# Performance work log

Measured on AMD Instinct MI355X. Metric: run time of the kernel, lower is better.

Reference implementation:

```python
import jax, jax.numpy as jnp
import numpy as np

B, N, T, D = 8, 64, 50, 4      # batch, atoms, timesteps, features per node
K, H = 2, 64                   # edge types, hidden (msg_hid = msg_out = n_hid)
START = 1                      # skip_first_edge_type=True
E = N * (N - 1)


def setup_inputs() -> dict:
    key = jax.random.key(0)
    ks = jax.random.split(key, 10)
    # fully-connected relation graph: all ordered pairs i != j
    recv_idx, send_idx = np.where(~np.eye(N, dtype=bool))
    eye = np.eye(N, dtype=np.float32)
    rel_rec = jnp.asarray(eye[recv_idx])    # [E, N] one-hot receivers
    rel_send = jnp.asarray(eye[send_idx])   # [E, N] one-hot senders
    s = 0.1
    return {
        "inputs": jax.random.normal(ks[0], (B, N, T, D), jnp.float32),
        "rel_type": jax.random.uniform(ks[1], (B, 1, E, K), jnp.float32),
        "rel_rec": rel_rec,
        "rel_send": rel_send,
        "fc1_w": jax.random.normal(ks[2], (K, H, 2 * D), jnp.float32) * s,
        "fc1_b": jnp.zeros((K, H), jnp.float32),
        "fc2_w": jax.random.normal(ks[3], (K, H, H), jnp.float32) * s,
        "fc2_b": jnp.zeros((K, H), jnp.float32),
        "out1_w": jax.random.normal(ks[4], (H, D + H), jnp.float32) * s,
        "out1_b": jnp.zeros((H,), jnp.float32),
        "out2_w": jax.random.normal(ks[5], (H, H), jnp.float32) * s,
        "out2_b": jnp.zeros((H,), jnp.float32),
        "out3_w": jax.random.normal(ks[6], (D, H), jnp.float32) * s,
        "out3_b": jnp.zeros((D,), jnp.float32),
        "pred_steps": 1,
    }


def reference(inputs, rel_type, rel_rec, rel_send,
              fc1_w, fc1_b, fc2_w, fc2_b,
              out1_w, out1_b, out2_w, out2_b, out3_w, out3_b,
              pred_steps):
    assert pred_steps == 1
    x_in = jnp.swapaxes(inputs, 1, 2)  # [B, T, N, D]
    t = x_in.shape[1]
    # rel_type [B,1,E,K] -> expand over time
    rt = jnp.broadcast_to(rel_type, (rel_type.shape[0], t) + rel_type.shape[2:])

    # node2edge: gather receivers/senders via one-hot matmuls
    recv = jnp.einsum('en,btnd->bted', rel_rec, x_in)
    send = jnp.einsum('en,btnd->bted', rel_send, x_in)
    pre_msg = jnp.concatenate([recv, send], axis=-1)  # [B,T,E,2D]

    # per-edge-type MLP, masked by inferred edge prob, accumulated
    all_msgs = jnp.zeros(pre_msg.shape[:3] + (H,), pre_msg.dtype)
    for i in range(START, K):
        h = jax.nn.relu(jnp.einsum('bted,hd->bteh', pre_msg, fc1_w[i]) + fc1_b[i])
        m = jax.nn.relu(jnp.einsum('bteh,oh->bteo', h, fc2_w[i]) + fc2_b[i])
        all_msgs = all_msgs + m * rt[..., i:i + 1]

    # edge2node: scatter-accumulate to receivers via one-hot transpose matmul
    agg = jnp.einsum('en,bteh->btnh', rel_rec, all_msgs)  # [B,T,N,H]

    aug = jnp.concatenate([x_in, agg], axis=-1)           # [B,T,N,D+H]
    h = jax.nn.relu(jnp.einsum('btni,oi->btno', aug, out1_w) + out1_b)
    h = jax.nn.relu(jnp.einsum('btni,oi->btno', h, out2_w) + out2_b)
    delta = jnp.einsum('btni,oi->btno', h, out3_w) + out3_b
    x_tp1 = x_in + delta                                  # predict_delta=True

    pred_all = x_tp1[:, :t - 1]                           # [B,T-1,N,D]
    return jnp.swapaxes(pred_all, 1, 2)                   # [B,N,T-1,D]
```

## Files before the change

kernel.cpp:

```cpp
#include <hip/hip_runtime.h>


#define NB 8
#define NN 64
#define NT 50
#define NTO 49
#define ND 4
#define NH 64
#define NE 4032

typedef _Float16 f16x8 __attribute__((ext_vector_type(8)));
typedef float f32x4 __attribute__((ext_vector_type(4)));

union Frag { unsigned u[4]; f16x8 f; };

__device__ __forceinline__ unsigned pk16(float lo, float hi) {
  return __builtin_bit_cast(unsigned, __builtin_amdgcn_cvt_pkrtz(lo, hi));
}

#define MFMA16(A, B, C) __builtin_amdgcn_mfma_f32_16x16x32_f16((A), (B), (C), 0, 0, 0)

__global__ __launch_bounds__(256) void nri_fused_kernel(
    const float* __restrict__ inputs,
    const float* __restrict__ rel_type,
    const float* __restrict__ fc1_w,
    const float* __restrict__ fc1_b,
    const float* __restrict__ fc2_w,
    const float* __restrict__ fc2_b,
    const float* __restrict__ out1_w,
    const float* __restrict__ out1_b,
    const float* __restrict__ out2_w,
    const float* __restrict__ out2_b,
    const float* __restrict__ out3_w,
    const float* __restrict__ out3_b,
    float* __restrict__ out)
{
  __shared__ float  Vl[NN * 68];
  __shared__ float  Pl[16 * 68];
  __shared__ float  Rl[16 * NN];
  __shared__ float4 Xl[16];
  __shared__ float  AggL[16 * 68];
  __shared__ float  H1L[16 * 68];
  __shared__ float  H2L[16 * 68];

  const int bid    = blockIdx.x;
  const int tile   = bid & 3;
  const int t      = (bid >> 2) % NTO;
  const int b      = bid / (4 * NTO);
  const int n_base = tile * 16;
  const int tid  = threadIdx.x;
  const int lane = tid & 63;
  const int w    = tid >> 6;
  const int q    = lane >> 4;
  const int r    = lane & 15;

  {
    const int k = lane;
    const float4 w1r = *(const float4*)(fc1_w + 512 + k * 8);
    const float4 w1s = *(const float4*)(fc1_w + 516 + k * 8);
    const float  b1k = fc1_b[64 + k];
    for (int i = w; i < NN; i += 4) {
      const float4 x = *(const float4*)(inputs + ((b * NN + i) * NT + t) * ND);
      Vl[i * 68 + k] = w1s.x * x.x + w1s.y * x.y + w1s.z * x.z + w1s.w * x.w;
    }
    for (int i = w; i < 16; i += 4) {
      const float4 x = *(const float4*)(inputs + ((b * NN + n_base + i) * NT + t) * ND);
      Pl[i * 68 + k] = b1k + w1r.x * x.x + w1r.y * x.y + w1r.z * x.z + w1r.w * x.w;
    }
  }
  for (int idx = tid; idx < 16 * NN; idx += 256) {
    const int i = idx >> 6, s = idx & 63;
    const int n = n_base + i;
    Rl[idx] = (s == n) ? 0.f
                       : rel_type[(b * NE + n * 63 + (s < n ? s : s - 1)) * 2 + 1];
  }
  if (tid < 16)
    Xl[tid] = *(const float4*)(inputs + ((b * NN + n_base + tid) * NT + t) * ND);

  Frag bfr[4][2];
  float b2l[4];
#pragma unroll
  for (int nt = 0; nt < 4; ++nt) {
    const int o = nt * 16 + r;
    b2l[nt] = fc2_b[64 + o];
#pragma unroll
    for (int ks = 0; ks < 2; ++ks) {
      const float* p = fc2_w + 4096 + o * 64 + ks * 32 + q * 8;
      const float4 c0 = *(const float4*)p;
      const float4 c1 = *(const float4*)(p + 4);
      bfr[nt][ks].u[0] = pk16(c0.x, c0.y);
      bfr[nt][ks].u[1] = pk16(c0.z, c0.w);
      bfr[nt][ks].u[2] = pk16(c1.x, c1.y);
      bfr[nt][ks].u[3] = pk16(c1.z, c1.w);
    }
  }
  __syncthreads();

#pragma unroll 1
  for (int np = 0; np < 4; ++np) {
    const int ni = w * 4 + np;
    float pn[16];
    *(float4*)(pn + 0)  = *(const float4*)(Pl + ni * 68 + q * 8);
    *(float4*)(pn + 4)  = *(const float4*)(Pl + ni * 68 + q * 8 + 4);
    *(float4*)(pn + 8)  = *(const float4*)(Pl + ni * 68 + 32 + q * 8);
    *(float4*)(pn + 12) = *(const float4*)(Pl + ni * 68 + 36 + q * 8);

    float ag0 = 0.f, ag1 = 0.f, ag2 = 0.f, ag3 = 0.f;
#pragma unroll
    for (int st = 0; st < 4; ++st) {
      const int s = st * 16 + r;
      float vv[16];
      *(float4*)(vv + 0)  = *(const float4*)(Vl + s * 68 + q * 8);
      *(float4*)(vv + 4)  = *(const float4*)(Vl + s * 68 + q * 8 + 4);
      *(float4*)(vv + 8)  = *(const float4*)(Vl + s * 68 + 32 + q * 8);
      *(float4*)(vv + 12) = *(const float4*)(Vl + s * 68 + 36 + q * 8);
      float h[16];
#pragma unroll
      for (int j = 0; j < 16; ++j) h[j] = fmaxf(pn[j] + vv[j], 0.f);
      Frag a0, a1;
      a0.u[0] = pk16(h[0],  h[1]);  a0.u[1] = pk16(h[2],  h[3]);
      a0.u[2] = pk16(h[4],  h[5]);  a0.u[3] = pk16(h[6],  h[7]);
      a1.u[0] = pk16(h[8],  h[9]);  a1.u[1] = pk16(h[10], h[11]);
      a1.u[2] = pk16(h[12], h[13]); a1.u[3] = pk16(h[14], h[15]);

      f32x4 d0 = {b2l[0], b2l[0], b2l[0], b2l[0]};
      f32x4 d1 = {b2l[1], b2l[1], b2l[1], b2l[1]};
      f32x4 d2 = {b2l[2], b2l[2], b2l[2], b2l[2]};
      f32x4 d3 = {b2l[3], b2l[3], b2l[3], b2l[3]};
      d0 = MFMA16(a0.f, bfr[0][0].f, d0); d0 = MFMA16(a1.f, bfr[0][1].f, d0);
      d1 = MFMA16(a0.f, bfr[1][0].f, d1); d1 = MFMA16(a1.f, bfr[1][1].f, d1);
      d2 = MFMA16(a0.f, bfr[2][0].f, d2); d2 = MFMA16(a1.f, bfr[2][1].f, d2);
      d3 = MFMA16(a0.f, bfr[3][0].f, d3); d3 = MFMA16(a1.f, bfr[3][1].f, d3);

      const float4 rt4 = *(const float4*)(Rl + ni * NN + st * 16 + q * 4);
      const float rte[4] = {rt4.x, rt4.y, rt4.z, rt4.w};
#pragma unroll
      for (int e = 0; e < 4; ++e) {
        ag0 = fmaf(rte[e], fmaxf(d0[e], 0.f), ag0);
        ag1 = fmaf(rte[e], fmaxf(d1[e], 0.f), ag1);
        ag2 = fmaf(rte[e], fmaxf(d2[e], 0.f), ag2);
        ag3 = fmaf(rte[e], fmaxf(d3[e], 0.f), ag3);
      }
    }
    ag0 += __shfl_xor(ag0, 16); ag0 += __shfl_xor(ag0, 32);
    ag1 += __shfl_xor(ag1, 16); ag1 += __shfl_xor(ag1, 32);
    ag2 += __shfl_xor(ag2, 16); ag2 += __shfl_xor(ag2, 32);
    ag3 += __shfl_xor(ag3, 16); ag3 += __shfl_xor(ag3, 32);
    const float val = (q == 0) ? ag0 : (q == 1) ? ag1 : (q == 2) ? ag2 : ag3;
    AggL[ni * 68 + lane] = val;
  }

  const int o = w * 16 + r;
  Frag B1[2], B2[2];
#pragma unroll
  for (int ks = 0; ks < 2; ++ks) {
    const float* p1 = out1_w + o * 68 + 4 + ks * 32 + q * 8;
    const float4 c0 = *(const float4*)p1;
    const float4 c1 = *(const float4*)(p1 + 4);
    B1[ks].u[0] = pk16(c0.x, c0.y); B1[ks].u[1] = pk16(c0.z, c0.w);
    B1[ks].u[2] = pk16(c1.x, c1.y); B1[ks].u[3] = pk16(c1.z, c1.w);
    const float* p2 = out2_w + o * 64 + ks * 32 + q * 8;
    const float4 e0 = *(const float4*)p2;
    const float4 e1 = *(const float4*)(p2 + 4);
    B2[ks].u[0] = pk16(e0.x, e0.y); B2[ks].u[1] = pk16(e0.z, e0.w);
    B2[ks].u[2] = pk16(e1.x, e1.y); B2[ks].u[3] = pk16(e1.z, e1.w);
  }
  const float4 w1x = *(const float4*)(out1_w + o * 68);
  const float b1o = out1_b[o];
  const float b2o = out2_b[o];
  __syncthreads();

  {
    Frag A[2];
#pragma unroll
    for (int ks = 0; ks < 2; ++ks) {
      const float4 g0 = *(const float4*)(AggL + r * 68 + ks * 32 + q * 8);
      const float4 g1 = *(const float4*)(AggL + r * 68 + ks * 32 + q * 8 + 4);
      A[ks].u[0] = pk16(g0.x, g0.y); A[ks].u[1] = pk16(g0.z, g0.w);
      A[ks].u[2] = pk16(g1.x, g1.y); A[ks].u[3] = pk16(g1.z, g1.w);
    }
    f32x4 d = {b1o, b1o, b1o, b1o};
    d = MFMA16(A[0].f, B1[0].f, d);
    d = MFMA16(A[1].f, B1[1].f, d);
#pragma unroll
    for (int reg = 0; reg < 4; ++reg) {
      const int n = q * 4 + reg;
      const float4 x = Xl[n];
      const float hv = d[reg] + x.x * w1x.x + x.y * w1x.y + x.z * w1x.z + x.w * w1x.w;
      H1L[n * 68 + o] = fmaxf(hv, 0.f);
    }
  }
  __syncthreads();

  {
    Frag A[2];
#pragma unroll
    for (int ks = 0; ks < 2; ++ks) {
      const float4 g0 = *(const float4*)(H1L + r * 68 + ks * 32 + q * 8);
      const float4 g1 = *(const float4*)(H1L + r * 68 + ks * 32 + q * 8 + 4);
      A[ks].u[0] = pk16(g0.x, g0.y); A[ks].u[1] = pk16(g0.z, g0.w);
      A[ks].u[2] = pk16(g1.x, g1.y); A[ks].u[3] = pk16(g1.z, g1.w);
    }
    f32x4 d = {b2o, b2o, b2o, b2o};
    d = MFMA16(A[0].f, B2[0].f, d);
    d = MFMA16(A[1].f, B2[1].f, d);
#pragma unroll
    for (int reg = 0; reg < 4; ++reg) {
      const int n = q * 4 + reg;
      H2L[n * 68 + o] = fmaxf(d[reg], 0.f);
    }
  }
  __syncthreads();

  if (w == 0) {
    Frag B3[2];
#pragma unroll
    for (int ks = 0; ks < 2; ++ks) {
      const float* p3 = out3_w + (r & 3) * 64 + ks * 32 + q * 8;
      float4 c0 = *(const float4*)p3;
      float4 c1 = *(const float4*)(p3 + 4);
      if (r >= 4) { c0 = make_float4(0, 0, 0, 0); c1 = make_float4(0, 0, 0, 0); }
      B3[ks].u[0] = pk16(c0.x, c0.y); B3[ks].u[1] = pk16(c0.z, c0.w);
      B3[ks].u[2] = pk16(c1.x, c1.y); B3[ks].u[3] = pk16(c1.z, c1.w);
    }
    Frag A[2];
#pragma unroll
    for (int ks = 0; ks < 2; ++ks) {
      const float4 g0 = *(const float4*)(H2L + r * 68 + ks * 32 + q * 8);
      const float4 g1 = *(const float4*)(H2L + r * 68 + ks * 32 + q * 8 + 4);
      A[ks].u[0] = pk16(g0.x, g0.y); A[ks].u[1] = pk16(g0.z, g0.w);
      A[ks].u[2] = pk16(g1.x, g1.y); A[ks].u[3] = pk16(g1.z, g1.w);
    }
    const float b3o = (r < 4) ? out3_b[r] : 0.f;
    f32x4 d = {b3o, b3o, b3o, b3o};
    d = MFMA16(A[0].f, B3[0].f, d);
    d = MFMA16(A[1].f, B3[1].f, d);
    if (r < 4) {
      const float* xf = (const float*)Xl;
#pragma unroll
      for (int reg = 0; reg < 4; ++reg) {
        const int n = q * 4 + reg;
        out[((b * NN + n_base + n) * NTO + t) * ND + r] = xf[n * 4 + r] + d[reg];
      }
    }
  }
}

extern "C" void kernel_launch(void* const* d_in, const int* in_sizes, int n_in,
                              void* d_out, int out_size, void* d_ws, size_t ws_size,
                              hipStream_t stream) {
  const float* inputs   = (const float*)d_in[0];
  const float* rel_type = (const float*)d_in[1];
  const float* fc1_w  = (const float*)d_in[4];
  const float* fc1_b  = (const float*)d_in[5];
  const float* fc2_w  = (const float*)d_in[6];
  const float* fc2_b  = (const float*)d_in[7];
  const float* out1_w = (const float*)d_in[8];
  const float* out1_b = (const float*)d_in[9];
  const float* out2_w = (const float*)d_in[10];
  const float* out2_b = (const float*)d_in[11];
  const float* out3_w = (const float*)d_in[12];
  const float* out3_b = (const float*)d_in[13];
  float* out = (float*)d_out;

  nri_fused_kernel<<<NB * NTO * 4, 256, 0, stream>>>(
      inputs, rel_type, fc1_w, fc1_b, fc2_w, fc2_b,
      out1_w, out1_b, out2_w, out2_b, out3_w, out3_b, out);
}
```

Measured before the change: 129.6 us.

## Split node tiles to 4 receivers per block and compute edge hidden in packed fp16

Each block now handles 4 receiver nodes instead of 16, so the grid is four times larger and each wave processes a single receiver with no inner node loop. The first-layer edge activations (sender and receiver projections) are stored in shared memory as fp16 and combined with packed half add and max, which removes the per-element float-to-half conversions. The cost is that every block recomputes the full 64-node sender projection and reloads the weights, four times as often as before. The output MLP now runs 16-row MFMAs with only 4 valid rows, and the fp16 sums add a little rounding error.

```diff
diff --git a/kernel.cpp b/kernel.cpp
--- a/kernel.cpp
+++ b/kernel.cpp
@@ -6,13 +6,13 @@
 #define NT 50
 #define NTO 49
 #define ND 4
-#define NH 64
 #define NE 4032
 
 typedef _Float16 f16x8 __attribute__((ext_vector_type(8)));
+typedef _Float16 f16x2 __attribute__((ext_vector_type(2)));
 typedef float f32x4 __attribute__((ext_vector_type(4)));
 
-union Frag { unsigned u[4]; f16x8 f; };
+union Frag8 { unsigned u[4]; f16x8 f; f16x2 h[4]; };
 
 __device__ __forceinline__ unsigned pk16(float lo, float hi) {
   return __builtin_bit_cast(unsigned, __builtin_amdgcn_cvt_pkrtz(lo, hi));
@@ -35,19 +35,19 @@
     const float* __restrict__ out3_b,
     float* __restrict__ out)
 {
-  __shared__ float  Vl[NN * 68];
-  __shared__ float  Pl[16 * 68];
-  __shared__ float  Rl[16 * NN];
-  __shared__ float4 Xl[16];
-  __shared__ float  AggL[16 * 68];
-  __shared__ float  H1L[16 * 68];
-  __shared__ float  H2L[16 * 68];
+  __shared__ _Float16 Vh[NN * 72];
+  __shared__ _Float16 Ph[4 * 72];
+  __shared__ float    Rl[4 * NN];
+  __shared__ float4   Xl[4];
+  __shared__ float    AggL[16 * 68];
+  __shared__ float    H1L[16 * 68];
+  __shared__ float    H2L[16 * 68];
 
   const int bid    = blockIdx.x;
-  const int tile   = bid & 3;
-  const int t      = (bid >> 2) % NTO;
-  const int b      = bid / (4 * NTO);
-  const int n_base = tile * 16;
+  const int tilei  = bid & 15;
+  const int t      = (bid >> 4) % NTO;
+  const int b      = bid / (16 * NTO);
+  const int n_base = tilei * 4;
   const int tid  = threadIdx.x;
   const int lane = tid & 63;
   const int w    = tid >> 6;
@@ -59,25 +59,27 @@
     const float4 w1r = *(const float4*)(fc1_w + 512 + k * 8);
     const float4 w1s = *(const float4*)(fc1_w + 516 + k * 8);
     const float  b1k = fc1_b[64 + k];
-    for (int i = w; i < NN; i += 4) {
+#pragma unroll 4
+    for (int i = w * 16; i < w * 16 + 16; ++i) {
       const float4 x = *(const float4*)(inputs + ((b * NN + i) * NT + t) * ND);
-      Vl[i * 68 + k] = w1s.x * x.x + w1s.y * x.y + w1s.z * x.z + w1s.w * x.w;
-    }
-    for (int i = w; i < 16; i += 4) {
-      const float4 x = *(const float4*)(inputs + ((b * NN + n_base + i) * NT + t) * ND);
-      Pl[i * 68 + k] = b1k + w1r.x * x.x + w1r.y * x.y + w1r.z * x.z + w1r.w * x.w;
-    }
-  }
-  for (int idx = tid; idx < 16 * NN; idx += 256) {
-    const int i = idx >> 6, s = idx & 63;
+      Vh[i * 72 + k] = (_Float16)(w1s.x*x.x + w1s.y*x.y + w1s.z*x.z + w1s.w*x.w);
+    }
+    {
+      const int n = n_base + w;
+      const float4 x = *(const float4*)(inputs + ((b * NN + n) * NT + t) * ND);
+      Ph[w * 72 + k] = (_Float16)(b1k + w1r.x*x.x + w1r.y*x.y + w1r.z*x.z + w1r.w*x.w);
+    }
+  }
+  {
+    const int i = w, s = lane;
     const int n = n_base + i;
-    Rl[idx] = (s == n) ? 0.f
-                       : rel_type[(b * NE + n * 63 + (s < n ? s : s - 1)) * 2 + 1];
-  }
-  if (tid < 16)
+    Rl[i * NN + s] = (s == n) ? 0.f
+                   : rel_type[(b * NE + n * 63 + (s < n ? s : s - 1)) * 2 + 1];
+  }
+  if (tid < 4)
     Xl[tid] = *(const float4*)(inputs + ((b * NN + n_base + tid) * NT + t) * ND);
 
-  Frag bfr[4][2];
+  Frag8 bfr[4][2];
   float b2l[4];
 #pragma unroll
   for (int nt = 0; nt < 4; ++nt) {
@@ -96,62 +98,57 @@
   }
   __syncthreads();
 
-#pragma unroll 1
-  for (int np = 0; np < 4; ++np) {
-    const int ni = w * 4 + np;
-    float pn[16];
-    *(float4*)(pn + 0)  = *(const float4*)(Pl + ni * 68 + q * 8);
-    *(float4*)(pn + 4)  = *(const float4*)(Pl + ni * 68 + q * 8 + 4);
-    *(float4*)(pn + 8)  = *(const float4*)(Pl + ni * 68 + 32 + q * 8);
-    *(float4*)(pn + 12) = *(const float4*)(Pl + ni * 68 + 36 + q * 8);
-
-    float ag0 = 0.f, ag1 = 0.f, ag2 = 0.f, ag3 = 0.f;
-#pragma unroll
-    for (int st = 0; st < 4; ++st) {
-      const int s = st * 16 + r;
-      float vv[16];
-      *(float4*)(vv + 0)  = *(const float4*)(Vl + s * 68 + q * 8);
-      *(float4*)(vv + 4)  = *(const float4*)(Vl + s * 68 + q * 8 + 4);
-      *(float4*)(vv + 8)  = *(const float4*)(Vl + s * 68 + 32 + q * 8);
-      *(float4*)(vv + 12) = *(const float4*)(Vl + s * 68 + 36 + q * 8);
-      float h[16];
-#pragma unroll
-      for (int j = 0; j < 16; ++j) h[j] = fmaxf(pn[j] + vv[j], 0.f);
-      Frag a0, a1;
-      a0.u[0] = pk16(h[0],  h[1]);  a0.u[1] = pk16(h[2],  h[3]);
-      a0.u[2] = pk16(h[4],  h[5]);  a0.u[3] = pk16(h[6],  h[7]);
-      a1.u[0] = pk16(h[8],  h[9]);  a1.u[1] = pk16(h[10], h[11]);
-      a1.u[2] = pk16(h[12], h[13]); a1.u[3] = pk16(h[14], h[15]);
-
-      f32x4 d0 = {b2l[0], b2l[0], b2l[0], b2l[0]};
-      f32x4 d1 = {b2l[1], b2l[1], b2l[1], b2l[1]};
-      f32x4 d2 = {b2l[2], b2l[2], b2l[2], b2l[2]};
-      f32x4 d3 = {b2l[3], b2l[3], b2l[3], b2l[3]};
-      d0 = MFMA16(a0.f, bfr[0][0].f, d0); d0 = MFMA16(a1.f, bfr[0][1].f, d0);
-      d1 = MFMA16(a0.f, bfr[1][0].f, d1); d1 = MFMA16(a1.f, bfr[1][1].f, d1);
-      d2 = MFMA16(a0.f, bfr[2][0].f, d2); d2 = MFMA16(a1.f, bfr[2][1].f, d2);
-      d3 = MFMA16(a0.f, bfr[3][0].f, d3); d3 = MFMA16(a1.f, bfr[3][1].f, d3);
-
-      const float4 rt4 = *(const float4*)(Rl + ni * NN + st * 16 + q * 4);
-      const float rte[4] = {rt4.x, rt4.y, rt4.z, rt4.w};
-#pragma unroll
-      for (int e = 0; e < 4; ++e) {
-        ag0 = fmaf(rte[e], fmaxf(d0[e], 0.f), ag0);
-        ag1 = fmaf(rte[e], fmaxf(d1[e], 0.f), ag1);
-        ag2 = fmaf(rte[e], fmaxf(d2[e], 0.f), ag2);
-        ag3 = fmaf(rte[e], fmaxf(d3[e], 0.f), ag3);
-      }
-    }
-    ag0 += __shfl_xor(ag0, 16); ag0 += __shfl_xor(ag0, 32);
-    ag1 += __shfl_xor(ag1, 16); ag1 += __shfl_xor(ag1, 32);
-    ag2 += __shfl_xor(ag2, 16); ag2 += __shfl_xor(ag2, 32);
-    ag3 += __shfl_xor(ag3, 16); ag3 += __shfl_xor(ag3, 32);
-    const float val = (q == 0) ? ag0 : (q == 1) ? ag1 : (q == 2) ? ag2 : ag3;
-    AggL[ni * 68 + lane] = val;
-  }
+  const int ni = w;
+  Frag8 pa0, pa1;
+  {
+    const _Float16* pp = Ph + ni * 72 + q * 8;
+    pa0.f = *(const f16x8*)pp;
+    pa1.f = *(const f16x8*)(pp + 32);
+  }
+
+  float ag0 = 0.f, ag1 = 0.f, ag2 = 0.f, ag3 = 0.f;
+#pragma unroll
+  for (int st = 0; st < 4; ++st) {
+    const int s = st * 16 + r;
+    const _Float16* vp = Vh + s * 72 + q * 8;
+    Frag8 va0, va1, a0, a1;
+    va0.f = *(const f16x8*)vp;
+    va1.f = *(const f16x8*)(vp + 32);
+    const f16x2 z = {(_Float16)0.f, (_Float16)0.f};
+#pragma unroll
+    for (int j = 0; j < 4; ++j) {
+      a0.h[j] = __builtin_elementwise_max((f16x2)(pa0.h[j] + va0.h[j]), z);
+      a1.h[j] = __builtin_elementwise_max((f16x2)(pa1.h[j] + va1.h[j]), z);
+    }
+
+    f32x4 d0 = {b2l[0], b2l[0], b2l[0], b2l[0]};
+    f32x4 d1 = {b2l[1], b2l[1], b2l[1], b2l[1]};
+    f32x4 d2 = {b2l[2], b2l[2], b2l[2], b2l[2]};
+    f32x4 d3 = {b2l[3], b2l[3], b2l[3], b2l[3]};
+    d0 = MFMA16(a0.f, bfr[0][0].f, d0); d0 = MFMA16(a1.f, bfr[0][1].f, d0);
+    d1 = MFMA16(a0.f, bfr[1][0].f, d1); d1 = MFMA16(a1.f, bfr[1][1].f, d1);
+    d2 = MFMA16(a0.f, bfr[2][0].f, d2); d2 = MFMA16(a1.f, bfr[2][1].f, d2);
+    d3 = MFMA16(a0.f, bfr[3][0].f, d3); d3 = MFMA16(a1.f, bfr[3][1].f, d3);
+
+    const float4 rt4 = *(const float4*)(Rl + ni * NN + st * 16 + q * 4);
+    const float rte[4] = {rt4.x, rt4.y, rt4.z, rt4.w};
+#pragma unroll
+    for (int e = 0; e < 4; ++e) {
+      ag0 = fmaf(rte[e], fmaxf(d0[e], 0.f), ag0);
+      ag1 = fmaf(rte[e], fmaxf(d1[e], 0.f), ag1);
+      ag2 = fmaf(rte[e], fmaxf(d2[e], 0.f), ag2);
+      ag3 = fmaf(rte[e], fmaxf(d3[e], 0.f), ag3);
+    }
+  }
+  ag0 += __shfl_xor(ag0, 16); ag0 += __shfl_xor(ag0, 32);
+  ag1 += __shfl_xor(ag1, 16); ag1 += __shfl_xor(ag1, 32);
+  ag2 += __shfl_xor(ag2, 16); ag2 += __shfl_xor(ag2, 32);
+  ag3 += __shfl_xor(ag3, 16); ag3 += __shfl_xor(ag3, 32);
+  const float aval = (q == 0) ? ag0 : (q == 1) ? ag1 : (q == 2) ? ag2 : ag3;
+  AggL[ni * 68 + lane] = aval;
 
   const int o = w * 16 + r;
-  Frag B1[2], B2[2];
+  Frag8 B1[2], B2[2];
 #pragma unroll
   for (int ks = 0; ks < 2; ++ks) {
     const float* p1 = out1_w + o * 68 + 4 + ks * 32 + q * 8;
@@ -171,76 +168,81 @@
   __syncthreads();
 
   {
-    Frag A[2];
-#pragma unroll
-    for (int ks = 0; ks < 2; ++ks) {
-      const float4 g0 = *(const float4*)(AggL + r * 68 + ks * 32 + q * 8);
-      const float4 g1 = *(const float4*)(AggL + r * 68 + ks * 32 + q * 8 + 4);
-      A[ks].u[0] = pk16(g0.x, g0.y); A[ks].u[1] = pk16(g0.z, g0.w);
-      A[ks].u[2] = pk16(g1.x, g1.y); A[ks].u[3] = pk16(g1.z, g1.w);
-    }
+    Frag8 A0, A1;
+    const float* gp = AggL + r * 68 + q * 8;
+    const float4 g0 = *(const float4*)gp;
+    const float4 g1 = *(const float4*)(gp + 4);
+    const float4 g2 = *(const float4*)(gp + 32);
+    const float4 g3 = *(const float4*)(gp + 36);
+    A0.u[0] = pk16(g0.x, g0.y); A0.u[1] = pk16(g0.z, g0.w);
+    A0.u[2] = pk16(g1.x, g1.y); A0.u[3] = pk16(g1.z, g1.w);
+    A1.u[0] = pk16(g2.x, g2.y); A1.u[1] = pk16(g2.z, g2.w);
+    A1.u[2] = pk16(g3.x, g3.y); A1.u[3] = pk16(g3.z, g3.w);
     f32x4 d = {b1o, b1o, b1o, b1o};
-    d = MFMA16(A[0].f, B1[0].f, d);
-    d = MFMA16(A[1].f, B1[1].f, d);
-#pragma unroll
-    for (int reg = 0; reg < 4; ++reg) {
-      const int n = q * 4 + reg;
-      const float4 x = Xl[n];
-      const float hv = d[reg] + x.x * w1x.x + x.y * w1x.y + x.z * w1x.z + x.w * w1x.w;
-      H1L[n * 68 + o] = fmaxf(hv, 0.f);
-    }
-  }
-  __syncthreads();
-
-  {
-    Frag A[2];
-#pragma unroll
-    for (int ks = 0; ks < 2; ++ks) {
-      const float4 g0 = *(const float4*)(H1L + r * 68 + ks * 32 + q * 8);
-      const float4 g1 = *(const float4*)(H1L + r * 68 + ks * 32 + q * 8 + 4);
-      A[ks].u[0] = pk16(g0.x, g0.y); A[ks].u[1] = pk16(g0.z, g0.w);
-      A[ks].u[2] = pk16(g1.x, g1.y); A[ks].u[3] = pk16(g1.z, g1.w);
-    }
+    d = MFMA16(A0.f, B1[0].f, d);
+    d = MFMA16(A1.f, B1[1].f, d);
+    if (q == 0) {
+#pragma unroll
+      for (int reg = 0; reg < 4; ++reg) {
+        const float4 x = Xl[reg];
+        const float hv = d[reg] + x.x*w1x.x + x.y*w1x.y + x.z*w1x.z + x.w*w1x.w;
+        H1L[reg * 68 + o] = fmaxf(hv, 0.f);
+      }
+    }
+  }
+  __syncthreads();
+
+  {
+    Frag8 A0, A1;
+    const float* gp = H1L + r * 68 + q * 8;
+    const float4 g0 = *(const float4*)gp;
+    const float4 g1 = *(const float4*)(gp + 4);
+    const float4 g2 = *(const float4*)(gp + 32);
+    const float4 g3 = *(const float4*)(gp + 36);
+    A0.u[0] = pk16(g0.x, g0.y); A0.u[1] = pk16(g0.z, g0.w);
+    A0.u[2] = pk16(g1.x, g1.y); A0.u[3] = pk16(g1.z, g1.w);
+    A1.u[0] = pk16(g2.x, g2.y); A1.u[1] = pk16(g2.z, g2.w);
+    A1.u[2] = pk16(g3.x, g3.y); A1.u[3] = pk16(g3.z, g3.w);
     f32x4 d = {b2o, b2o, b2o, b2o};
-    d = MFMA16(A[0].f, B2[0].f, d);
-    d = MFMA16(A[1].f, B2[1].f, d);
-#pragma unroll
-    for (int reg = 0; reg < 4; ++reg) {
-      const int n = q * 4 + reg;
-      H2L[n * 68 + o] = fmaxf(d[reg], 0.f);
+    d = MFMA16(A0.f, B2[0].f, d);
+    d = MFMA16(A1.f, B2[1].f, d);
+    if (q == 0) {
+#pragma unroll
+      for (int reg = 0; reg < 4; ++reg)
+        H2L[reg * 68 + o] = fmaxf(d[reg], 0.f);
     }
   }
   __syncthreads();
 
   if (w == 0) {
-    Frag B3[2];
+    Frag8 B3[2];
 #pragma unroll
     for (int ks = 0; ks < 2; ++ks) {
       const float* p3 = out3_w + (r & 3) * 64 + ks * 32 + q * 8;
-      float4 c0 = *(const float4*)p3;
-      float4 c1 = *(const float4*)(p3 + 4);
-      if (r >= 4) { c0 = make_float4(0, 0, 0, 0); c1 = make_float4(0, 0, 0, 0); }
+      const float4 c0 = *(const float4*)p3;
+      const float4 c1 = *(const float4*)(p3 + 4);
       B3[ks].u[0] = pk16(c0.x, c0.y); B3[ks].u[1] = pk16(c0.z, c0.w);
       B3[ks].u[2] = pk16(c1.x, c1.y); B3[ks].u[3] = pk16(c1.z, c1.w);
     }
-    Frag A[2];
-#pragma unroll
-    for (int ks = 0; ks < 2; ++ks) {
-      const float4 g0 = *(const float4*)(H2L + r * 68 + ks * 32 + q * 8);
-      const float4 g1 = *(const float4*)(H2L + r * 68 + ks * 32 + q * 8 + 4);
-      A[ks].u[0] = pk16(g0.x, g0.y); A[ks].u[1] = pk16(g0.z, g0.w);
-      A[ks].u[2] = pk16(g1.x, g1.y); A[ks].u[3] = pk16(g1.z, g1.w);
-    }
-    const float b3o = (r < 4) ? out3_b[r] : 0.f;
+    Frag8 A0, A1;
+    const float* gp = H2L + r * 68 + q * 8;
+    const float4 g0 = *(const float4*)gp;
+    const float4 g1 = *(const float4*)(gp + 4);
+    const float4 g2 = *(const float4*)(gp + 32);
+    const float4 g3 = *(const float4*)(gp + 36);
+    A0.u[0] = pk16(g0.x, g0.y); A0.u[1] = pk16(g0.z, g0.w);
+    A0.u[2] = pk16(g1.x, g1.y); A0.u[3] = pk16(g1.z, g1.w);
+    A1.u[0] = pk16(g2.x, g2.y); A1.u[1] = pk16(g2.z, g2.w);
+    A1.u[2] = pk16(g3.x, g3.y); A1.u[3] = pk16(g3.z, g3.w);
+    const float b3o = out3_b[r & 3];
     f32x4 d = {b3o, b3o, b3o, b3o};
-    d = MFMA16(A[0].f, B3[0].f, d);
-    d = MFMA16(A[1].f, B3[1].f, d);
-    if (r < 4) {
+    d = MFMA16(A0.f, B3[0].f, d);
+    d = MFMA16(A1.f, B3[1].f, d);
+    if (q == 0 && r < 4) {
       const float* xf = (const float*)Xl;
 #pragma unroll
       for (int reg = 0; reg < 4; ++reg) {
-        const int n = q * 4 + reg;
-        out[((b * NN + n_base + n) * NTO + t) * ND + r] = xf[n * 4 + r] + d[reg];
+        out[((b * NN + n_base + reg) * NTO + t) * ND + r] = xf[reg * 4 + r] + d[reg];
       }
     }
   }
@@ -263,7 +265,7 @@
   const float* out3_b = (const float*)d_in[13];
   float* out = (float*)d_out;
 
-  nri_fused_kernel<<<NB * NTO * 4, 256, 0, stream>>>(
+  nri_fused_kernel<<<NB * NTO * 16, 256, 0, stream>>>(
       inputs, rel_type, fc1_w, fc1_b, fc2_w, fc2_b,
       out1_w, out1_b, out2_w, out2_b, out3_w, out3_b, out);
 }
```

Result: slower. 163.0 us (+25.8%).
